# Kernel optimization log

Hardware: AMD Instinct MI355X
Metric: run time of the kernel (lower is better)

Reference implementation:

```python
import jax, jax.numpy as jnp
import numpy as np

N_NODES = 50000
N_EDGES = 1600000
D = 128
L = 4
N_GRAPHS = 512


def setup_inputs() -> dict:
    key = jax.random.key(0)
    ks = jax.random.split(key, 8)
    x = jax.random.normal(ks[0], (N_NODES, D), dtype=jnp.float32)
    edge_index = jax.random.randint(ks[1], (2, N_EDGES), 0, N_NODES, dtype=jnp.int64)
    batch = jnp.sort(jax.random.randint(ks[2], (N_NODES,), 0, N_GRAPHS, dtype=jnp.int64))
    # MLP params per GIN layer: Linear(D->D), ReLU, Linear(D->D). Stacked over L layers.
    s = 1.0 / np.sqrt(D)
    Ws1 = jax.random.uniform(ks[3], (L, D, D), jnp.float32, -s, s)
    bs1 = jax.random.uniform(ks[4], (L, D), jnp.float32, -s, s)
    Ws2 = jax.random.uniform(ks[5], (L, D, D), jnp.float32, -s, s)
    bs2 = jax.random.uniform(ks[6], (L, D), jnp.float32, -s, s)
    return {"x": x, "edge_index": edge_index, "batch": batch,
            "Ws1": Ws1, "bs1": bs1, "Ws2": Ws2, "bs2": bs2}


def reference(x, edge_index, batch, Ws1, bs1, Ws2, bs2):
    src, dst = edge_index[0], edge_index[1]
    for l in range(L):
        # GINConv (eps=0): h = MLP(x + sum_{j in N(i)} x_j)
        agg = jax.ops.segment_sum(x[src], dst, num_segments=N_NODES)  # [N, D]
        h = x + agg
        h = jax.nn.relu(h @ Ws1[l] + bs1[l])
        x = h @ Ws2[l] + bs2[l]
    # global_add_pool: segment-sum node features by graph id
    return jax.ops.segment_sum(x, batch, num_segments=N_GRAPHS)  # [G, D]
```

## Files before the change

kernel.cpp:

```cpp
#include <hip/hip_runtime.h>

#define NN 50000
#define NE 1600000
#define DD 128
#define NL 4
#define NG 512
#define NBUK 196
#define NBLK 196
#define EPB 8192
#define HN (NBUK * NBLK)
#define HT 151

typedef __attribute__((ext_vector_type(8))) short short8;
typedef __attribute__((ext_vector_type(4))) float floatx4;

__device__ __forceinline__ unsigned short f2bf(float f) {
    unsigned int u = __float_as_uint(f);
    u += 0x7fffu + ((u >> 16) & 1u);
    return (unsigned short)(u >> 16);
}
__device__ __forceinline__ float bf2f(unsigned short u) {
    return __uint_as_float(((unsigned int)u) << 16);
}

__global__ __launch_bounds__(256) void cvt_kernel(const float* __restrict__ x,
                                                  unsigned short* __restrict__ xbf) {
    int idx = blockIdx.x * 256 + threadIdx.x;
    float4 f = ((const float4*)x)[idx];
    ushort4 o;
    o.x = f2bf(f.x); o.y = f2bf(f.y); o.z = f2bf(f.z); o.w = f2bf(f.w);
    ((ushort4*)xbf)[idx] = o;
}


__global__ __launch_bounds__(512) void bhist_kernel(const int* __restrict__ dst,
                                                    int* __restrict__ hist) {
    __shared__ int h[NBUK];
    int tid = threadIdx.x;
    for (int i = tid; i < NBUK; i += 512) h[i] = 0;
    __syncthreads();
    int base = blockIdx.x * EPB;
#pragma unroll
    for (int it = 0; it < EPB / 512; it++) {
        int e = base + it * 512 + tid;
        if (e < NE) atomicAdd(&h[dst[e] >> 8], 1);
    }
    __syncthreads();
    for (int i = tid; i < NBUK; i += 512) hist[i * NBLK + blockIdx.x] = h[i];
}

__global__ __launch_bounds__(256) void sum_tiles_kernel(const int* __restrict__ in,
                                                        int* __restrict__ tsum, int n) {
    int i = blockIdx.x * 256 + threadIdx.x;
    __shared__ int s[256];
    s[threadIdx.x] = (i < n) ? in[i] : 0;
    __syncthreads();
    for (int off = 128; off > 0; off >>= 1) {
        if (threadIdx.x < off) s[threadIdx.x] += s[threadIdx.x + off];
        __syncthreads();
    }
    if (threadIdx.x == 0) tsum[blockIdx.x] = s[0];
}

__global__ __launch_bounds__(256) void scan_tiles_kernel(const int* __restrict__ tsum,
                                                         int* __restrict__ toff, int ntiles) {
    int t = threadIdx.x;
    __shared__ int s[256];
    int v = (t < ntiles) ? tsum[t] : 0;
    s[t] = v;
    __syncthreads();
    for (int off = 1; off < 256; off <<= 1) {
        int u = (t >= off) ? s[t - off] : 0;
        __syncthreads();
        s[t] += u;
        __syncthreads();
    }
    if (t < ntiles) toff[t] = s[t] - v;
}

__global__ __launch_bounds__(256) void scan_out_kernel(const int* __restrict__ in,
                                                       const int* __restrict__ toff,
                                                       int* __restrict__ out, int n) {
    int i = blockIdx.x * 256 + threadIdx.x;
    int t = threadIdx.x;
    int v = (i < n) ? in[i] : 0;
    __shared__ int s[256];
    s[t] = v;
    __syncthreads();
    for (int off = 1; off < 256; off <<= 1) {
        int u = (t >= off) ? s[t - off] : 0;
        __syncthreads();
        s[t] += u;
        __syncthreads();
    }
    if (i < n) out[i] = toff[blockIdx.x] + s[t] - v;
}

__global__ __launch_bounds__(512) void bscatter_kernel(const int* __restrict__ src,
                                                       const int* __restrict__ dst,
                                                       const int* __restrict__ bkoff,
                                                       int* __restrict__ ebuf) {
    __shared__ int h[NBUK];
    int tid = threadIdx.x;
    for (int i = tid; i < NBUK; i += 512) h[i] = 0;
    __syncthreads();
    int base = blockIdx.x * EPB;
#pragma unroll
    for (int it = 0; it < EPB / 512; it++) {
        int e = base + it * 512 + tid;
        if (e < NE) {
            int d = dst[e];
            int bu = d >> 8;
            int p = atomicAdd(&h[bu], 1);
            ebuf[bkoff[bu * NBLK + blockIdx.x] + p] = (src[e] << 8) | (d & 255);
        }
    }
}

__global__ __launch_bounds__(256) void bucket_csr_kernel(const int* __restrict__ ebuf,
                                                         const int* __restrict__ bkoff,
                                                         int* __restrict__ rowptr,
                                                         int* __restrict__ col) {
    __shared__ int cnt[256], exc[256], c2[256];
    int b = blockIdx.x, tid = threadIdx.x;
    int segstart = bkoff[b * NBLK];
    int segend = (b < NBUK - 1) ? bkoff[(b + 1) * NBLK] : NE;
    cnt[tid] = 0;
    c2[tid] = 0;
    __syncthreads();
    for (int i = segstart + tid; i < segend; i += 256)
        atomicAdd(&cnt[ebuf[i] & 255], 1);
    __syncthreads();
    int v = cnt[tid];
    exc[tid] = v;
    __syncthreads();
    for (int off = 1; off < 256; off <<= 1) {
        int u = (tid >= off) ? exc[tid - off] : 0;
        __syncthreads();
        exc[tid] += u;
        __syncthreads();
    }
    int excl = exc[tid] - v;
    exc[tid] = excl;
    int node = (b << 8) + tid;
    if (node <= NN) rowptr[node] = segstart + excl;
    __syncthreads();
    for (int i = segstart + tid; i < segend; i += 256) {
        int ev = ebuf[i];
        int low = ev & 255;
        int p = atomicAdd(&c2[low], 1);
        col[segstart + exc[low] + p] = ((unsigned)ev) >> 8;
    }
}

__global__ __launch_bounds__(256) void prep_kernel(const float* __restrict__ Ws1,
                                                   const float* __restrict__ Ws2,
                                                   unsigned short* __restrict__ W1T,
                                                   unsigned short* __restrict__ W2T) {
    int idx = blockIdx.x * 256 + threadIdx.x;
    int l = idx >> 14;
    int rem = idx & 16383;
    int k = rem >> 7;
    int n = rem & 127;
    int o = (l << 14) + (n << 7) + k;
    W1T[o] = f2bf(Ws1[idx]);
    W2T[o] = f2bf(Ws2[idx]);
}

__global__ __launch_bounds__(256) void agg_kernel(const unsigned short* __restrict__ xbf,
                                                  const int* __restrict__ rowptr,
                                                  const int* __restrict__ col,
                                                  unsigned short* __restrict__ hpre) {
    int g = threadIdx.x >> 4;
    int lane = threadIdx.x & 15;
    int node = blockIdx.x * 16 + g;
    const uint4* base = (const uint4*)xbf;
    float a[8];
    {
        uint4 v = base[node * 16 + lane];
        a[0] = __uint_as_float(v.x << 16); a[1] = __uint_as_float(v.x & 0xFFFF0000u);
        a[2] = __uint_as_float(v.y << 16); a[3] = __uint_as_float(v.y & 0xFFFF0000u);
        a[4] = __uint_as_float(v.z << 16); a[5] = __uint_as_float(v.z & 0xFFFF0000u);
        a[6] = __uint_as_float(v.w << 16); a[7] = __uint_as_float(v.w & 0xFFFF0000u);
    }
    int s = rowptr[node], e = rowptr[node + 1];
    int i = s;
    for (; i + 8 <= e; i += 8) {
        uint4 v0 = base[col[i] * 16 + lane];
        uint4 v1 = base[col[i + 1] * 16 + lane];
        uint4 v2 = base[col[i + 2] * 16 + lane];
        uint4 v3 = base[col[i + 3] * 16 + lane];
        uint4 v4 = base[col[i + 4] * 16 + lane];
        uint4 v5 = base[col[i + 5] * 16 + lane];
        uint4 v6 = base[col[i + 6] * 16 + lane];
        uint4 v7 = base[col[i + 7] * 16 + lane];
#define ACC(V)                                                            \
        a[0] += __uint_as_float(V.x << 16); a[1] += __uint_as_float(V.x & 0xFFFF0000u); \
        a[2] += __uint_as_float(V.y << 16); a[3] += __uint_as_float(V.y & 0xFFFF0000u); \
        a[4] += __uint_as_float(V.z << 16); a[5] += __uint_as_float(V.z & 0xFFFF0000u); \
        a[6] += __uint_as_float(V.w << 16); a[7] += __uint_as_float(V.w & 0xFFFF0000u)
        ACC(v0); ACC(v1); ACC(v2); ACC(v3); ACC(v4); ACC(v5); ACC(v6); ACC(v7);
    }
    for (; i < e; i++) {
        uint4 v = base[col[i] * 16 + lane];
        ACC(v);
    }
#undef ACC
    uint4 o;
    o.x = (unsigned int)f2bf(a[0]) | ((unsigned int)f2bf(a[1]) << 16);
    o.y = (unsigned int)f2bf(a[2]) | ((unsigned int)f2bf(a[3]) << 16);
    o.z = (unsigned int)f2bf(a[4]) | ((unsigned int)f2bf(a[5]) << 16);
    o.w = (unsigned int)f2bf(a[6]) | ((unsigned int)f2bf(a[7]) << 16);
    ((uint4*)hpre)[node * 16 + lane] = o;
}

#define WS_STR 136
template <bool RELU>
__global__ __launch_bounds__(256) void gemm_kernel(const unsigned short* __restrict__ A,
                                                   const unsigned short* __restrict__ WT,
                                                   const float* __restrict__ bias,
                                                   unsigned short* __restrict__ O) {
    __shared__ unsigned short Ws[64 * WS_STR];
    int bx = blockIdx.x;
    int m = bx >> 1, nh = bx & 1;
    int tid = threadIdx.x;

    const uint4* wg = (const uint4*)(WT + (size_t)(nh * 64) * DD);
#pragma unroll
    for (int it = 0; it < 4; it++) {
        int idx = it * 256 + tid;
        int n = idx >> 4, kc = idx & 15;
        *(uint4*)&Ws[n * WS_STR + kc * 8] = wg[idx];
    }
    __syncthreads();

    int w = tid >> 6;
    int lane = tid & 63;
    int quad = lane >> 4;
    int li = lane & 15;
    int rowb = m * 128 + w * 32;

    floatx4 acc[2][4];
#pragma unroll
    for (int mi = 0; mi < 2; mi++)
#pragma unroll
        for (int tn = 0; tn < 4; tn++) acc[mi][tn] = (floatx4){0.f, 0.f, 0.f, 0.f};

#pragma unroll
    for (int kk = 0; kk < 4; kk++) {
        int k0 = kk * 32 + quad * 8;
        short8 af[2];
#pragma unroll
        for (int mi = 0; mi < 2; mi++) {
            int ar = rowb + mi * 16 + li;
            af[mi] = (ar < NN) ? *(const short8*)(A + (size_t)ar * DD + k0)
                               : (short8){0, 0, 0, 0, 0, 0, 0, 0};
        }
#pragma unroll
        for (int tn = 0; tn < 4; tn++) {
            short8 bf = *(const short8*)&Ws[(tn * 16 + li) * WS_STR + k0];
            acc[0][tn] = __builtin_amdgcn_mfma_f32_16x16x32_bf16(af[0], bf, acc[0][tn], 0, 0, 0);
            acc[1][tn] = __builtin_amdgcn_mfma_f32_16x16x32_bf16(af[1], bf, acc[1][tn], 0, 0, 0);
        }
    }
#pragma unroll
    for (int tn = 0; tn < 4; tn++) {
        int colg = nh * 64 + tn * 16 + li;
        float bv = bias[colg];
#pragma unroll
        for (int mi = 0; mi < 2; mi++) {
#pragma unroll
            for (int r = 0; r < 4; r++) {
                int grow = rowb + mi * 16 + quad * 4 + r;
                if (grow < NN) {
                    float v = acc[mi][tn][r] + bv;
                    if (RELU) v = fmaxf(v, 0.f);
                    O[(size_t)grow * DD + colg] = f2bf(v);
                }
            }
        }
    }
}

__global__ __launch_bounds__(128) void pool_kernel(const unsigned short* __restrict__ x,
                                                   const int* __restrict__ batch,
                                                   float* __restrict__ out) {
    int g = blockIdx.x;
    int lo = 0, hi = NN;
    while (lo < hi) { int mid = (lo + hi) >> 1; if (batch[mid] < g) lo = mid + 1; else hi = mid; }
    int s = lo;
    hi = NN;
    while (lo < hi) { int mid = (lo + hi) >> 1; if (batch[mid] < g + 1) lo = mid + 1; else hi = mid; }
    int e = lo;
    int d = threadIdx.x;
    float acc = 0.f;
    for (int i = s; i < e; i++) acc += bf2f(x[(size_t)i * DD + d]);
    out[g * DD + d] = acc;
}

extern "C" void kernel_launch(void* const* d_in, const int* in_sizes, int n_in,
                              void* d_out, int out_size, void* d_ws, size_t ws_size,
                              hipStream_t stream) {
    const float* x0 = (const float*)d_in[0];
    const int* edge = (const int*)d_in[1];
    const int* batch = (const int*)d_in[2];
    const float* Ws1 = (const float*)d_in[3];
    const float* bs1 = (const float*)d_in[4];
    const float* Ws2 = (const float*)d_in[5];
    const float* bs2 = (const float*)d_in[6];
    float* out = (float*)d_out;
    const int* src = edge;
    const int* dst = edge + NE;

    char* ws = (char*)d_ws;
    size_t off = 0;
    auto alloc = [&](size_t bytes) {
        void* p = ws + off;
        off += (bytes + 255) & ~(size_t)255;
        return p;
    };
    unsigned short* x0bf = (unsigned short*)alloc((size_t)NN * DD * 2);
    unsigned short* xA = (unsigned short*)alloc((size_t)NN * DD * 2);
    unsigned short* xB = (unsigned short*)alloc((size_t)NN * DD * 2);
    unsigned short* hpre = (unsigned short*)alloc((size_t)NN * DD * 2);
    unsigned short* Hbuf = (unsigned short*)alloc((size_t)NN * DD * 2);
    int* col = (int*)alloc((size_t)NE * 4);
    int* ebuf = (int*)alloc((size_t)NE * 4);
    int* hist = (int*)alloc((size_t)HN * 4);
    int* bkoff = (int*)alloc((size_t)HN * 4);
    int* tsum = (int*)alloc((size_t)HT * 4);
    int* toff = (int*)alloc((size_t)HT * 4);
    int* rowptr = (int*)alloc((size_t)(NN + 1) * 4);
    unsigned short* W1T = (unsigned short*)alloc((size_t)NL * DD * DD * 2);
    unsigned short* W2T = (unsigned short*)alloc((size_t)NL * DD * DD * 2);

    cvt_kernel<<<(NN * DD / 4) / 256, 256, 0, stream>>>(x0, x0bf);
    bhist_kernel<<<NBLK, 512, 0, stream>>>(dst, hist);
    sum_tiles_kernel<<<HT, 256, 0, stream>>>(hist, tsum, HN);
    scan_tiles_kernel<<<1, 256, 0, stream>>>(tsum, toff, HT);
    scan_out_kernel<<<HT, 256, 0, stream>>>(hist, toff, bkoff, HN);
    bscatter_kernel<<<NBLK, 512, 0, stream>>>(src, dst, bkoff, ebuf);
    bucket_csr_kernel<<<NBUK, 256, 0, stream>>>(ebuf, bkoff, rowptr, col);
    prep_kernel<<<(NL * DD * DD) / 256, 256, 0, stream>>>(Ws1, Ws2, W1T, W2T);

    const unsigned short* xin = x0bf;
    unsigned short* bufs[2] = {xA, xB};
    const int gemm_grid = ((NN + 127) / 128) * 2;
    for (int l = 0; l < NL; l++) {
        agg_kernel<<<NN / 16, 256, 0, stream>>>(xin, rowptr, col, hpre);
        unsigned short* xout = bufs[l & 1];
        gemm_kernel<true><<<gemm_grid, 256, 0, stream>>>(hpre, W1T + l * DD * DD,
                                                         bs1 + l * DD, Hbuf);
        gemm_kernel<false><<<gemm_grid, 256, 0, stream>>>(Hbuf, W2T + l * DD * DD,
                                                          bs2 + l * DD, xout);
        xin = xout;
    }
    pool_kernel<<<NG, 128, 0, stream>>>(xin, batch, out);
}
```

Measured before the change: 494.7 us.

## Split node features into column slices so aggregation gathers from cache-resident slices

Node features are stored as four 32-column bf16 slices, each a contiguous NN×32 array. Aggregation runs as four passes, one per slice, so each pass gathers from a 3.2 MB working set that can stay in L2/LLC instead of the full 12.8 MB table. The GEMM, conversion and pooling kernels are rewritten to read and write this sliced layout. In exchange there are four times as many aggregation launches, each re-reading rowptr/col, and the GEMM output stores become more scattered.

```diff
diff --git a/kernel.cpp b/kernel.cpp
--- a/kernel.cpp
+++ b/kernel.cpp
@@ -10,6 +10,7 @@
 #define EPB 8192
 #define HN (NBUK * NBLK)
 #define HT 151
+#define SLICE ((size_t)NN * 32)
 
 typedef __attribute__((ext_vector_type(8))) short short8;
 typedef __attribute__((ext_vector_type(4))) float floatx4;
@@ -24,12 +25,19 @@
 }
 
 __global__ __launch_bounds__(256) void cvt_kernel(const float* __restrict__ x,
-                                                  unsigned short* __restrict__ xbf) {
-    int idx = blockIdx.x * 256 + threadIdx.x;
-    float4 f = ((const float4*)x)[idx];
-    ushort4 o;
-    o.x = f2bf(f.x); o.y = f2bf(f.y); o.z = f2bf(f.z); o.w = f2bf(f.w);
-    ((ushort4*)xbf)[idx] = o;
+                                                  unsigned short* __restrict__ xcs) {
+    int t = blockIdx.x * 256 + threadIdx.x;
+    int node = t >> 4, chunk = t & 15;
+    int pass = chunk >> 2, sub = chunk & 3;
+    const float* xp = x + (size_t)node * DD + chunk * 8;
+    float4 f0 = *(const float4*)xp;
+    float4 f1 = *(const float4*)(xp + 4);
+    uint4 o;
+    o.x = (unsigned int)f2bf(f0.x) | ((unsigned int)f2bf(f0.y) << 16);
+    o.y = (unsigned int)f2bf(f0.z) | ((unsigned int)f2bf(f0.w) << 16);
+    o.z = (unsigned int)f2bf(f1.x) | ((unsigned int)f2bf(f1.y) << 16);
+    o.w = (unsigned int)f2bf(f1.z) | ((unsigned int)f2bf(f1.w) << 16);
+    *(uint4*)(xcs + (size_t)pass * SLICE + (size_t)node * 32 + sub * 8) = o;
 }
 
 
@@ -167,17 +175,18 @@
     W2T[o] = f2bf(Ws2[idx]);
 }
 
-__global__ __launch_bounds__(256) void agg_kernel(const unsigned short* __restrict__ xbf,
-                                                  const int* __restrict__ rowptr,
-                                                  const int* __restrict__ col,
-                                                  unsigned short* __restrict__ hpre) {
-    int g = threadIdx.x >> 4;
-    int lane = threadIdx.x & 15;
-    int node = blockIdx.x * 16 + g;
-    const uint4* base = (const uint4*)xbf;
+__global__ __launch_bounds__(256) void agg_cs_kernel(const unsigned short* __restrict__ xcs,
+                                                     const int* __restrict__ rowptr,
+                                                     const int* __restrict__ col,
+                                                     unsigned short* __restrict__ hcs,
+                                                     int pass) {
+    int node = blockIdx.x * 64 + (threadIdx.x >> 2);
+    int lane = threadIdx.x & 3;
+    if (node >= NN) return;
+    const uint4* base = (const uint4*)(xcs + (size_t)pass * SLICE);
     float a[8];
     {
-        uint4 v = base[node * 16 + lane];
+        uint4 v = base[node * 4 + lane];
         a[0] = __uint_as_float(v.x << 16); a[1] = __uint_as_float(v.x & 0xFFFF0000u);
         a[2] = __uint_as_float(v.y << 16); a[3] = __uint_as_float(v.y & 0xFFFF0000u);
         a[4] = __uint_as_float(v.z << 16); a[5] = __uint_as_float(v.z & 0xFFFF0000u);
@@ -186,14 +195,14 @@
     int s = rowptr[node], e = rowptr[node + 1];
     int i = s;
     for (; i + 8 <= e; i += 8) {
-        uint4 v0 = base[col[i] * 16 + lane];
-        uint4 v1 = base[col[i + 1] * 16 + lane];
-        uint4 v2 = base[col[i + 2] * 16 + lane];
-        uint4 v3 = base[col[i + 3] * 16 + lane];
-        uint4 v4 = base[col[i + 4] * 16 + lane];
-        uint4 v5 = base[col[i + 5] * 16 + lane];
-        uint4 v6 = base[col[i + 6] * 16 + lane];
-        uint4 v7 = base[col[i + 7] * 16 + lane];
+        uint4 v0 = base[col[i] * 4 + lane];
+        uint4 v1 = base[col[i + 1] * 4 + lane];
+        uint4 v2 = base[col[i + 2] * 4 + lane];
+        uint4 v3 = base[col[i + 3] * 4 + lane];
+        uint4 v4 = base[col[i + 4] * 4 + lane];
+        uint4 v5 = base[col[i + 5] * 4 + lane];
+        uint4 v6 = base[col[i + 6] * 4 + lane];
+        uint4 v7 = base[col[i + 7] * 4 + lane];
 #define ACC(V)                                                            \
         a[0] += __uint_as_float(V.x << 16); a[1] += __uint_as_float(V.x & 0xFFFF0000u); \
         a[2] += __uint_as_float(V.y << 16); a[3] += __uint_as_float(V.y & 0xFFFF0000u); \
@@ -202,7 +211,7 @@
         ACC(v0); ACC(v1); ACC(v2); ACC(v3); ACC(v4); ACC(v5); ACC(v6); ACC(v7);
     }
     for (; i < e; i++) {
-        uint4 v = base[col[i] * 16 + lane];
+        uint4 v = base[col[i] * 4 + lane];
         ACC(v);
     }
 #undef ACC
@@ -211,7 +220,7 @@
     o.y = (unsigned int)f2bf(a[2]) | ((unsigned int)f2bf(a[3]) << 16);
     o.z = (unsigned int)f2bf(a[4]) | ((unsigned int)f2bf(a[5]) << 16);
     o.w = (unsigned int)f2bf(a[6]) | ((unsigned int)f2bf(a[7]) << 16);
-    ((uint4*)hpre)[node * 16 + lane] = o;
+    ((uint4*)(hcs + (size_t)pass * SLICE))[node * 4 + lane] = o;
 }
 
 #define WS_STR 136
@@ -253,8 +262,9 @@
 #pragma unroll
         for (int mi = 0; mi < 2; mi++) {
             int ar = rowb + mi * 16 + li;
-            af[mi] = (ar < NN) ? *(const short8*)(A + (size_t)ar * DD + k0)
-                               : (short8){0, 0, 0, 0, 0, 0, 0, 0};
+            af[mi] = (ar < NN)
+                ? *(const short8*)(A + (size_t)kk * SLICE + (size_t)ar * 32 + quad * 8)
+                : (short8){0, 0, 0, 0, 0, 0, 0, 0};
         }
 #pragma unroll
         for (int tn = 0; tn < 4; tn++) {
@@ -262,11 +272,13 @@
             acc[0][tn] = __builtin_amdgcn_mfma_f32_16x16x32_bf16(af[0], bf, acc[0][tn], 0, 0, 0);
             acc[1][tn] = __builtin_amdgcn_mfma_f32_16x16x32_bf16(af[1], bf, acc[1][tn], 0, 0, 0);
         }
+        (void)k0;
     }
 #pragma unroll
     for (int tn = 0; tn < 4; tn++) {
         int colg = nh * 64 + tn * 16 + li;
         float bv = bias[colg];
+        size_t obase = (size_t)(colg >> 5) * SLICE + (colg & 31);
 #pragma unroll
         for (int mi = 0; mi < 2; mi++) {
 #pragma unroll
@@ -275,7 +287,7 @@
                 if (grow < NN) {
                     float v = acc[mi][tn][r] + bv;
                     if (RELU) v = fmaxf(v, 0.f);
-                    O[(size_t)grow * DD + colg] = f2bf(v);
+                    O[obase + (size_t)grow * 32] = f2bf(v);
                 }
             }
         }
@@ -293,8 +305,9 @@
     while (lo < hi) { int mid = (lo + hi) >> 1; if (batch[mid] < g + 1) lo = mid + 1; else hi = mid; }
     int e = lo;
     int d = threadIdx.x;
+    size_t base = (size_t)(d >> 5) * SLICE + (d & 31);
     float acc = 0.f;
-    for (int i = s; i < e; i++) acc += bf2f(x[(size_t)i * DD + d]);
+    for (int i = s; i < e; i++) acc += bf2f(x[base + (size_t)i * 32]);
     out[g * DD + d] = acc;
 }
 
@@ -334,7 +347,7 @@
     unsigned short* W1T = (unsigned short*)alloc((size_t)NL * DD * DD * 2);
     unsigned short* W2T = (unsigned short*)alloc((size_t)NL * DD * DD * 2);
 
-    cvt_kernel<<<(NN * DD / 4) / 256, 256, 0, stream>>>(x0, x0bf);
+    cvt_kernel<<<(NN * 16) / 256, 256, 0, stream>>>(x0, x0bf);
     bhist_kernel<<<NBLK, 512, 0, stream>>>(dst, hist);
     sum_tiles_kernel<<<HT, 256, 0, stream>>>(hist, tsum, HN);
     scan_tiles_kernel<<<1, 256, 0, stream>>>(tsum, toff, HT);
@@ -345,9 +358,11 @@
 
     const unsigned short* xin = x0bf;
     unsigned short* bufs[2] = {xA, xB};
+    const int agg_grid = (NN + 63) / 64;
     const int gemm_grid = ((NN + 127) / 128) * 2;
     for (int l = 0; l < NL; l++) {
-        agg_kernel<<<NN / 16, 256, 0, stream>>>(xin, rowptr, col, hpre);
+        for (int p = 0; p < 4; p++)
+            agg_cs_kernel<<<agg_grid, 256, 0, stream>>>(xin, rowptr, col, hpre, p);
         unsigned short* xout = bufs[l & 1];
         gemm_kernel<true><<<gemm_grid, 256, 0, stream>>>(hpre, W1T + l * DD * DD,
                                                          bs1 + l * DD, Hbuf);
```

Measured after the change: 549.9 us. 1.11x slower.
